# Performance work log

Hardware: AMD Instinct MI355X
Metric: run time of the kernel (lower is better)

The kernel has to match this reference:

```python
import jax, jax.numpy as jnp
import numpy as np

ALPHA = 0.2  # LeakyReLU negative slope
NEG_INF = -9e15


def setup_inputs() -> dict:
    key = jax.random.key(0)
    k1, k2, k3, k4 = jax.random.split(key, 4)
    B, N, F_in, F_out = 8, 2048, 512, 256
    h = jax.random.normal(k1, (B, N, F_in), dtype=jnp.float32)
    adj = jax.random.randint(k2, (B, N, N), 0, 2, dtype=jnp.int32)
    W = jax.random.normal(k3, (F_in, F_out), dtype=jnp.float32) * (1.414 / np.sqrt(F_in))
    a = jax.random.normal(k4, (2 * F_out, 1), dtype=jnp.float32) * (1.414 / np.sqrt(2 * F_out))
    return {"h": h, "adj": adj, "W": W, "a": a}


def reference(h, adj, W, a):
    # Wh: [B, N, F_out]
    Wh = jnp.matmul(h, W)
    F_out = W.shape[1]
    a1 = a[:F_out, 0]   # [F_out] -> source (row i) part
    a2 = a[F_out:, 0]   # [F_out] -> target (col j) part
    # e[b,i,j] = leakyrelu(Wh[b,i]@a1 + Wh[b,j]@a2)  (decomposed concat-attention)
    f1 = jnp.einsum('bnf,f->bn', Wh, a1)  # [B, N]
    f2 = jnp.einsum('bnf,f->bn', Wh, a2)  # [B, N]
    e = f1[:, :, None] + f2[:, None, :]   # [B, N, N]
    e = jnp.where(e > 0, e, ALPHA * e)    # LeakyReLU
    e = jnp.where(adj > 0, e, NEG_INF)
    attention = jax.nn.softmax(e, axis=2)
    # dropout p=0.0 / eval mode: identity
    h_prime = jnp.matmul(attention, Wh)   # [B, N, F_out]
    return jax.nn.elu(h_prime)            # concat=True branch
```

## Files before the change

### kernel.cpp

```cpp
#include <hip/hip_runtime.h>
#include <hip/hip_bf16.h>

#define GAT_ALPHA 0.2f

typedef short bf16x8 __attribute__((ext_vector_type(8)));
typedef float f32x4 __attribute__((ext_vector_type(4)));

__device__ __forceinline__ unsigned f2bf_u(float x) {
  union { float f; unsigned u; } v; v.f = x;
  return (v.u + 0x7fffu + ((v.u >> 16) & 1u)) >> 16;
}
__device__ __forceinline__ unsigned short f2bf(float x) { return (unsigned short)f2bf_u(x); }

__global__ void k_wt(const float* __restrict__ W, unsigned short* __restrict__ WT) {
  int kb = blockIdx.x * 8;
  int f = threadIdx.x;
  bf16x8 o;
#pragma unroll
  for (int i = 0; i < 8; ++i) o[i] = (short)f2bf(W[(kb + i) * 256 + f]);
  *reinterpret_cast<bf16x8*>(WT + f * 512 + kb) = o;
}

__global__ __launch_bounds__(256, 4) void k_gemm1(
    const float* __restrict__ h, const unsigned short* __restrict__ WT,
    const float* __restrict__ avec,
    unsigned short* __restrict__ WhT,
    float* __restrict__ E1p, float* __restrict__ E1n,
    float* __restrict__ E2p, float* __restrict__ E2n)
{
  const int bx = blockIdx.x;
  const int b = bx & 7, ng = bx >> 3;
  const int n0 = ng * 32;
  const int t = threadIdx.x;
  const int lane = t & 63, w = t >> 6;
  const int l15 = lane & 15, q = lane >> 4;

  __shared__ __align__(16) unsigned short Wt[256 * 36];
  __shared__ float f1a[32], f2a[32];
  if (t < 32) { f1a[t] = 0.f; f2a[t] = 0.f; }

  f32x4 acc[4][2];
#pragma unroll
  for (int i = 0; i < 4; ++i)
#pragma unroll
    for (int j = 0; j < 2; ++j) acc[i][j] = (f32x4){0.f, 0.f, 0.f, 0.f};

  const size_t hbase = ((size_t)(b * 2048 + n0)) * 512;

#pragma unroll 2
  for (int k0 = 0; k0 < 512; k0 += 32) {
    bf16x8 af[4];
#pragma unroll
    for (int mt = 0; mt < 4; ++mt)
      af[mt] = *reinterpret_cast<const bf16x8*>(WT + (w * 64 + mt * 16 + l15) * 512 + k0 + q * 8);
    bf16x8 bfr[2];
#pragma unroll
    for (int nt = 0; nt < 2; ++nt) {
      const float* hp = h + hbase + (size_t)(nt * 16 + l15) * 512 + k0 + q * 8;
      float4 x0 = *reinterpret_cast<const float4*>(hp);
      float4 x1 = *reinterpret_cast<const float4*>(hp + 4);
      bf16x8 bb;
      bb[0] = (short)f2bf(x0.x); bb[1] = (short)f2bf(x0.y);
      bb[2] = (short)f2bf(x0.z); bb[3] = (short)f2bf(x0.w);
      bb[4] = (short)f2bf(x1.x); bb[5] = (short)f2bf(x1.y);
      bb[6] = (short)f2bf(x1.z); bb[7] = (short)f2bf(x1.w);
      bfr[nt] = bb;
    }
#pragma unroll
    for (int mt = 0; mt < 4; ++mt)
#pragma unroll
      for (int nt = 0; nt < 2; ++nt)
        acc[mt][nt] = __builtin_amdgcn_mfma_f32_16x16x32_bf16(af[mt], bfr[nt], acc[mt][nt], 0, 0, 0);
  }

  float s1[2] = {0.f, 0.f}, s2[2] = {0.f, 0.f};
#pragma unroll
  for (int mt = 0; mt < 4; ++mt) {
#pragma unroll
    for (int nt = 0; nt < 2; ++nt) {
#pragma unroll
      for (int r = 0; r < 4; ++r) {
        int f = w * 64 + mt * 16 + q * 4 + r;
        float v = acc[mt][nt][r];
        Wt[f * 36 + nt * 16 + l15] = f2bf(v);
        s1[nt] += v * avec[f];
        s2[nt] += v * avec[256 + f];
      }
    }
  }
#pragma unroll
  for (int nt = 0; nt < 2; ++nt) {
    s1[nt] += __shfl_xor(s1[nt], 16); s1[nt] += __shfl_xor(s1[nt], 32);
    s2[nt] += __shfl_xor(s2[nt], 16); s2[nt] += __shfl_xor(s2[nt], 32);
  }
  __syncthreads();
  if (q == 0) {
#pragma unroll
    for (int nt = 0; nt < 2; ++nt) {
      atomicAdd(&f1a[nt * 16 + l15], s1[nt]);
      atomicAdd(&f2a[nt * 16 + l15], s2[nt]);
    }
  }
#pragma unroll
  for (int i = 0; i < 8; ++i) {
    int f = i * 32 + (t >> 3), g = t & 7;
    uint2 v = *reinterpret_cast<const uint2*>(Wt + f * 36 + g * 4);
    *reinterpret_cast<uint2*>(WhT + (size_t)(b * 256 + f) * 2048 + n0 + g * 4) = v;
  }
  __syncthreads();
  if (t < 32) {
    int n = b * 2048 + n0 + t;
    float f1 = f1a[t], f2 = f2a[t];
    E1p[n] = __expf(f1);
    E1n[n] = __expf(GAT_ALPHA * f1);
    E2p[n] = __expf(f2);
    E2n[n] = __expf(GAT_ALPHA * f2);
  }
}

__device__ __forceinline__ void build_frag(
    unsigned short* dst, int4 alo, int4 ahi, float e1p, float e1n,
    float4 epl, float4 eph, float4 enl, float4 enh, float& den)
{
  float p0 = alo.x ? fmaxf(e1p * epl.x, e1n * enl.x) : 0.f;
  float p1 = alo.y ? fmaxf(e1p * epl.y, e1n * enl.y) : 0.f;
  float p2 = alo.z ? fmaxf(e1p * epl.z, e1n * enl.z) : 0.f;
  float p3 = alo.w ? fmaxf(e1p * epl.w, e1n * enl.w) : 0.f;
  float p4 = ahi.x ? fmaxf(e1p * eph.x, e1n * enh.x) : 0.f;
  float p5 = ahi.y ? fmaxf(e1p * eph.y, e1n * enh.y) : 0.f;
  float p6 = ahi.z ? fmaxf(e1p * eph.z, e1n * enh.z) : 0.f;
  float p7 = ahi.w ? fmaxf(e1p * eph.w, e1n * enh.w) : 0.f;
  den += ((p0 + p1) + (p2 + p3)) + ((p4 + p5) + (p6 + p7));
  uint4 pk;
  pk.x = f2bf_u(p0) | (f2bf_u(p1) << 16);
  pk.y = f2bf_u(p2) | (f2bf_u(p3) << 16);
  pk.z = f2bf_u(p4) | (f2bf_u(p5) << 16);
  pk.w = f2bf_u(p6) | (f2bf_u(p7) << 16);
  *reinterpret_cast<uint4*>(dst) = pk;
}

template<int JS>
__global__ __launch_bounds__(512, 4) void k_gat(
    const int* __restrict__ adj, const unsigned short* __restrict__ WhT,
    const float* __restrict__ E1p, const float* __restrict__ E1n,
    const float* __restrict__ E2p, const float* __restrict__ E2n,
    float* __restrict__ num0, float* __restrict__ num1, float* __restrict__ denp)
{
  const int NCH = 16 / JS;
  const int bx = blockIdx.x;
  const int b = bx & 7;
  const int rest = bx >> 3;
  const int js = (JS == 2) ? (rest & 1) : 0;
  const int ig = (JS == 2) ? (rest >> 1) : rest;
  const int i0 = ig * 64;
  const int j00 = js * (NCH * 128);

  const int t = threadIdx.x;
  const int lane = t & 63, w = t >> 6;
  const int l15 = lane & 15, q = lane >> 4;
  const int m = t & 15, qk = (t >> 4) & 3, pp = t >> 6;
  const int rt0 = pp >> 2, ks = pp & 3;
  const int r0 = rt0 * 16 + m, r1 = r0 + 32;
  const int cb = ks * 32 + qk * 8;

  __shared__ __align__(16) unsigned short Pb[2][8192];
  __shared__ float den_l[64];
  if (t < 64) den_l[t] = 0.f;

  const float e1p0 = E1p[b * 2048 + i0 + r0], e1n0 = E1n[b * 2048 + i0 + r0];
  const float e1p1 = E1p[b * 2048 + i0 + r1], e1n1 = E1n[b * 2048 + i0 + r1];
  float d0 = 0.f, d1 = 0.f;

  f32x4 acc[4][2];
#pragma unroll
  for (int i = 0; i < 4; ++i)
#pragma unroll
    for (int j = 0; j < 2; ++j) acc[i][j] = (f32x4){0.f, 0.f, 0.f, 0.f};

  const size_t adj0 = ((size_t)(b * 2048 + i0 + r0)) * 2048 + j00 + cb;
  const size_t adj1 = adj0 + (size_t)32 * 2048;
  const int e2b = b * 2048 + j00 + cb;
  const unsigned short* Wb = WhT + (size_t)(b * 256 + w * 32) * 2048 + j00;

  {
    int4 a0l = *reinterpret_cast<const int4*>(adj + adj0);
    int4 a0h = *reinterpret_cast<const int4*>(adj + adj0 + 4);
    int4 a1l = *reinterpret_cast<const int4*>(adj + adj1);
    int4 a1h = *reinterpret_cast<const int4*>(adj + adj1 + 4);
    float4 epl = *reinterpret_cast<const float4*>(E2p + e2b);
    float4 eph = *reinterpret_cast<const float4*>(E2p + e2b + 4);
    float4 enl = *reinterpret_cast<const float4*>(E2n + e2b);
    float4 enh = *reinterpret_cast<const float4*>(E2n + e2b + 4);
    build_frag(&Pb[0][(pp * 64 + lane) * 8], a0l, a0h, e1p0, e1n0, epl, eph, enl, enh, d0);
    build_frag(&Pb[0][((pp + 8) * 64 + lane) * 8], a1l, a1h, e1p1, e1n1, epl, eph, enl, enh, d1);
  }

  for (int c = 0; c < NCH; ++c) {
    __syncthreads();
    int4 na0l, na0h, na1l, na1h;
    if (c + 1 < NCH) {
      int o = (c + 1) * 128;
      na0l = *reinterpret_cast<const int4*>(adj + adj0 + o);
      na0h = *reinterpret_cast<const int4*>(adj + adj0 + o + 4);
      na1l = *reinterpret_cast<const int4*>(adj + adj1 + o);
      na1h = *reinterpret_cast<const int4*>(adj + adj1 + o + 4);
    }
    bf16x8 bfr[2][4];
#pragma unroll
    for (int ct = 0; ct < 2; ++ct)
#pragma unroll
      for (int k2 = 0; k2 < 4; ++k2)
        bfr[ct][k2] = *reinterpret_cast<const bf16x8*>(
            Wb + (size_t)(ct * 16 + l15) * 2048 + c * 128 + k2 * 32 + q * 8);
    const unsigned short* pb = &Pb[c & 1][0];
#pragma unroll
    for (int k2 = 0; k2 < 4; ++k2) {
      bf16x8 afr[4];
#pragma unroll
      for (int rt = 0; rt < 4; ++rt)
        afr[rt] = *reinterpret_cast<const bf16x8*>(pb + ((rt * 4 + k2) * 64 + lane) * 8);
#pragma unroll
      for (int rt = 0; rt < 4; ++rt)
#pragma unroll
        for (int ct = 0; ct < 2; ++ct)
          acc[rt][ct] = __builtin_amdgcn_mfma_f32_16x16x32_bf16(afr[rt], bfr[ct][k2], acc[rt][ct], 0, 0, 0);
    }
    if (c + 1 < NCH) {
      int o = (c + 1) * 128;
      float4 epl = *reinterpret_cast<const float4*>(E2p + e2b + o);
      float4 eph = *reinterpret_cast<const float4*>(E2p + e2b + o + 4);
      float4 enl = *reinterpret_cast<const float4*>(E2n + e2b + o);
      float4 enh = *reinterpret_cast<const float4*>(E2n + e2b + o + 4);
      unsigned short* wb = &Pb[(c + 1) & 1][0];
      build_frag(wb + (pp * 64 + lane) * 8, na0l, na0h, e1p0, e1n0, epl, eph, enl, enh, d0);
      build_frag(wb + ((pp + 8) * 64 + lane) * 8, na1l, na1h, e1p1, e1n1, epl, eph, enl, enh, d1);
    }
  }

  d0 += __shfl_xor(d0, 16); d0 += __shfl_xor(d0, 32);
  d1 += __shfl_xor(d1, 16); d1 += __shfl_xor(d1, 32);
  if (lane < 16) {
    atomicAdd(&den_l[r0], d0);
    atomicAdd(&den_l[r1], d1);
  }
  __syncthreads();

  float* nout = (JS == 2 && js == 1) ? num1 : num0;
#pragma unroll
  for (int rt = 0; rt < 4; ++rt) {
#pragma unroll
    for (int r = 0; r < 4; ++r) {
      int row = rt * 16 + q * 4 + r;
      size_t ob = ((size_t)(b * 2048 + i0 + row)) * 256 + w * 32;
#pragma unroll
      for (int ct = 0; ct < 2; ++ct)
        nout[ob + ct * 16 + l15] = acc[rt][ct][r];
    }
  }
  if (t < 64) denp[js * 16384 + b * 2048 + i0 + t] = den_l[t];
}

template<int JS>
__global__ __launch_bounds__(256) void k_fin(
    const float* __restrict__ n0p, const float* __restrict__ n1p,
    const float* __restrict__ denp, float* __restrict__ out)
{
  int i = blockIdx.x * 256 + threadIdx.x;
#pragma unroll
  for (int rep = 0; rep < 2; ++rep) {
    int i4 = i + rep * 524288;
    float4 v = reinterpret_cast<const float4*>(n0p)[i4];
    float dn = denp[i4 >> 6];
    if (JS == 2) {
      float4 u = reinterpret_cast<const float4*>(n1p)[i4];
      v.x += u.x; v.y += u.y; v.z += u.z; v.w += u.w;
      dn += denp[16384 + (i4 >> 6)];
    }
    float id = 1.0f / dn;
    float4 o;
    float x;
    x = v.x * id; o.x = x > 0.f ? x : (__expf(x) - 1.f);
    x = v.y * id; o.y = x > 0.f ? x : (__expf(x) - 1.f);
    x = v.z * id; o.z = x > 0.f ? x : (__expf(x) - 1.f);
    x = v.w * id; o.w = x > 0.f ? x : (__expf(x) - 1.f);
    reinterpret_cast<float4*>(out)[i4] = o;
  }
}

extern "C" void kernel_launch(void* const* d_in, const int* in_sizes, int n_in,
                              void* d_out, int out_size, void* d_ws, size_t ws_size,
                              hipStream_t stream) {
  const float* h   = (const float*)d_in[0];
  const int*   adj = (const int*)d_in[1];
  const float* W   = (const float*)d_in[2];
  const float* a   = (const float*)d_in[3];
  float* out = (float*)d_out;

  char* ws = (char*)d_ws;
  unsigned short* WhT = (unsigned short*)ws;
  unsigned short* WT  = (unsigned short*)(ws + 8388608);
  float* E1p  = (float*)(ws + 8388608 + 262144);
  float* E1n  = E1p + 16384;
  float* E2p  = E1n + 16384;
  float* E2n  = E2p + 16384;
  float* denp = E2n + 16384;
  float* num1 = denp + 2 * 16384;

  const size_t need2 = 8388608ull + 262144 + 4 * 65536 + 131072 + 16777216;
  const bool js2 = (ws_size >= need2);

  k_wt<<<dim3(64), dim3(256), 0, stream>>>(W, WT);
  k_gemm1<<<dim3(512), dim3(256), 0, stream>>>(h, WT, a, WhT, E1p, E1n, E2p, E2n);
  if (js2) {
    k_gat<2><<<dim3(512), dim3(512), 0, stream>>>(adj, WhT, E1p, E1n, E2p, E2n, out, num1, denp);
    k_fin<2><<<dim3(2048), dim3(256), 0, stream>>>(out, num1, denp, out);
  } else {
    k_gat<1><<<dim3(256), dim3(512), 0, stream>>>(adj, WhT, E1p, E1n, E2p, E2n, out, num1, denp);
    k_fin<1><<<dim3(2048), dim3(256), 0, stream>>>(out, num1, denp, out);
  }
}
```

Before: 284.6 us.

## Drop split-K GAT path, fuse normalize+ELU epilogue, deepen register prefetch pipelines

The gemm1 loop is rewritten as a fully unrolled register-prefetch pipeline: WT is loaded one step ahead and h two steps ahead. The GAT kernel drops the two-way column split and the separate finalize kernel. Softmax normalization and ELU now run in its epilogue, which saves one launch and the partial-sum round trip through global memory. Its adj/E2 loads are prefetched two chunks ahead and the WhT fragments one chunk ahead. The cost is a grid of only 256 blocks, lower occupancy hints and higher register pressure, which could leave the GPU underfilled.

Measured after the change: 262.3 us. 1.09x faster.

```diff
diff --git a/kernel.cpp b/kernel.cpp
--- a/kernel.cpp
+++ b/kernel.cpp
@@ -21,7 +21,7 @@
   *reinterpret_cast<bf16x8*>(WT + f * 512 + kb) = o;
 }
 
-__global__ __launch_bounds__(256, 4) void k_gemm1(
+__global__ __launch_bounds__(256, 2) void k_gemm1(
     const float* __restrict__ h, const unsigned short* __restrict__ WT,
     const float* __restrict__ avec,
     unsigned short* __restrict__ WhT,
@@ -46,19 +46,41 @@
     for (int j = 0; j < 2; ++j) acc[i][j] = (f32x4){0.f, 0.f, 0.f, 0.f};
 
   const size_t hbase = ((size_t)(b * 2048 + n0)) * 512;
-
-#pragma unroll 2
-  for (int k0 = 0; k0 < 512; k0 += 32) {
-    bf16x8 af[4];
-#pragma unroll
-    for (int mt = 0; mt < 4; ++mt)
-      af[mt] = *reinterpret_cast<const bf16x8*>(WT + (w * 64 + mt * 16 + l15) * 512 + k0 + q * 8);
+  const unsigned short* wtb = WT + (w * 64 + l15) * 512 + q * 8;
+  const float* hrow0 = h + hbase + (size_t)l15 * 512 + q * 8;
+  const float* hrow1 = h + hbase + (size_t)(16 + l15) * 512 + q * 8;
+
+  bf16x8 afA[4], afN[4];
+  float4 hA[4], hB[4], hN[4];
+#pragma unroll
+  for (int mt = 0; mt < 4; ++mt) afA[mt] = *reinterpret_cast<const bf16x8*>(wtb + mt * 16 * 512);
+  hA[0] = *reinterpret_cast<const float4*>(hrow0);
+  hA[1] = *reinterpret_cast<const float4*>(hrow0 + 4);
+  hA[2] = *reinterpret_cast<const float4*>(hrow1);
+  hA[3] = *reinterpret_cast<const float4*>(hrow1 + 4);
+  hB[0] = *reinterpret_cast<const float4*>(hrow0 + 32);
+  hB[1] = *reinterpret_cast<const float4*>(hrow0 + 36);
+  hB[2] = *reinterpret_cast<const float4*>(hrow1 + 32);
+  hB[3] = *reinterpret_cast<const float4*>(hrow1 + 36);
+
+#pragma unroll
+  for (int k = 0; k < 16; ++k) {
+    if (k < 15) {
+      const unsigned short* p = wtb + (k + 1) * 32;
+#pragma unroll
+      for (int mt = 0; mt < 4; ++mt) afN[mt] = *reinterpret_cast<const bf16x8*>(p + mt * 16 * 512);
+    }
+    if (k < 14) {
+      int o = (k + 2) * 32;
+      hN[0] = *reinterpret_cast<const float4*>(hrow0 + o);
+      hN[1] = *reinterpret_cast<const float4*>(hrow0 + o + 4);
+      hN[2] = *reinterpret_cast<const float4*>(hrow1 + o);
+      hN[3] = *reinterpret_cast<const float4*>(hrow1 + o + 4);
+    }
     bf16x8 bfr[2];
 #pragma unroll
     for (int nt = 0; nt < 2; ++nt) {
-      const float* hp = h + hbase + (size_t)(nt * 16 + l15) * 512 + k0 + q * 8;
-      float4 x0 = *reinterpret_cast<const float4*>(hp);
-      float4 x1 = *reinterpret_cast<const float4*>(hp + 4);
+      float4 x0 = hA[nt * 2], x1 = hA[nt * 2 + 1];
       bf16x8 bb;
       bb[0] = (short)f2bf(x0.x); bb[1] = (short)f2bf(x0.y);
       bb[2] = (short)f2bf(x0.z); bb[3] = (short)f2bf(x0.w);
@@ -70,7 +92,15 @@
     for (int mt = 0; mt < 4; ++mt)
 #pragma unroll
       for (int nt = 0; nt < 2; ++nt)
-        acc[mt][nt] = __builtin_amdgcn_mfma_f32_16x16x32_bf16(af[mt], bfr[nt], acc[mt][nt], 0, 0, 0);
+        acc[mt][nt] = __builtin_amdgcn_mfma_f32_16x16x32_bf16(afA[mt], bfr[nt], acc[mt][nt], 0, 0, 0);
+    if (k < 15) {
+#pragma unroll
+      for (int mt = 0; mt < 4; ++mt) afA[mt] = afN[mt];
+#pragma unroll
+      for (int i = 0; i < 4; ++i) hA[i] = hB[i];
+#pragma unroll
+      for (int i = 0; i < 4; ++i) hB[i] = hN[i];
+    }
   }
 
   float s1[2] = {0.f, 0.f}, s2[2] = {0.f, 0.f};
@@ -139,22 +169,15 @@
   *reinterpret_cast<uint4*>(dst) = pk;
 }
 
-template<int JS>
-__global__ __launch_bounds__(512, 4) void k_gat(
+__global__ __launch_bounds__(512, 2) void k_gat(
     const int* __restrict__ adj, const unsigned short* __restrict__ WhT,
     const float* __restrict__ E1p, const float* __restrict__ E1n,
     const float* __restrict__ E2p, const float* __restrict__ E2n,
-    float* __restrict__ num0, float* __restrict__ num1, float* __restrict__ denp)
+    float* __restrict__ out)
 {
-  const int NCH = 16 / JS;
   const int bx = blockIdx.x;
-  const int b = bx & 7;
-  const int rest = bx >> 3;
-  const int js = (JS == 2) ? (rest & 1) : 0;
-  const int ig = (JS == 2) ? (rest >> 1) : rest;
+  const int b = bx & 7, ig = bx >> 3;
   const int i0 = ig * 64;
-  const int j00 = js * (NCH * 128);
-
   const int t = threadIdx.x;
   const int lane = t & 63, w = t >> 6;
   const int l15 = lane & 15, q = lane >> 4;
@@ -177,41 +200,61 @@
 #pragma unroll
     for (int j = 0; j < 2; ++j) acc[i][j] = (f32x4){0.f, 0.f, 0.f, 0.f};
 
-  const size_t adj0 = ((size_t)(b * 2048 + i0 + r0)) * 2048 + j00 + cb;
+  const size_t adj0 = ((size_t)(b * 2048 + i0 + r0)) * 2048 + cb;
   const size_t adj1 = adj0 + (size_t)32 * 2048;
-  const int e2b = b * 2048 + j00 + cb;
-  const unsigned short* Wb = WhT + (size_t)(b * 256 + w * 32) * 2048 + j00;
-
-  {
-    int4 a0l = *reinterpret_cast<const int4*>(adj + adj0);
-    int4 a0h = *reinterpret_cast<const int4*>(adj + adj0 + 4);
-    int4 a1l = *reinterpret_cast<const int4*>(adj + adj1);
-    int4 a1h = *reinterpret_cast<const int4*>(adj + adj1 + 4);
-    float4 epl = *reinterpret_cast<const float4*>(E2p + e2b);
-    float4 eph = *reinterpret_cast<const float4*>(E2p + e2b + 4);
-    float4 enl = *reinterpret_cast<const float4*>(E2n + e2b);
-    float4 enh = *reinterpret_cast<const float4*>(E2n + e2b + 4);
-    build_frag(&Pb[0][(pp * 64 + lane) * 8], a0l, a0h, e1p0, e1n0, epl, eph, enl, enh, d0);
-    build_frag(&Pb[0][((pp + 8) * 64 + lane) * 8], a1l, a1h, e1p1, e1n1, epl, eph, enl, enh, d1);
-  }
-
-  for (int c = 0; c < NCH; ++c) {
-    __syncthreads();
-    int4 na0l, na0h, na1l, na1h;
-    if (c + 1 < NCH) {
-      int o = (c + 1) * 128;
-      na0l = *reinterpret_cast<const int4*>(adj + adj0 + o);
-      na0h = *reinterpret_cast<const int4*>(adj + adj0 + o + 4);
-      na1l = *reinterpret_cast<const int4*>(adj + adj1 + o);
-      na1h = *reinterpret_cast<const int4*>(adj + adj1 + o + 4);
-    }
-    bf16x8 bfr[2][4];
-#pragma unroll
-    for (int ct = 0; ct < 2; ++ct)
-#pragma unroll
-      for (int k2 = 0; k2 < 4; ++k2)
-        bfr[ct][k2] = *reinterpret_cast<const bf16x8*>(
-            Wb + (size_t)(ct * 16 + l15) * 2048 + c * 128 + k2 * 32 + q * 8);
+  const int e2b = b * 2048 + cb;
+  const unsigned short* Wb = WhT + (size_t)(b * 256 + w * 32) * 2048;
+
+  int4 z0l = *reinterpret_cast<const int4*>(adj + adj0);
+  int4 z0h = *reinterpret_cast<const int4*>(adj + adj0 + 4);
+  int4 z1l = *reinterpret_cast<const int4*>(adj + adj1);
+  int4 z1h = *reinterpret_cast<const int4*>(adj + adj1 + 4);
+  float4 zpl = *reinterpret_cast<const float4*>(E2p + e2b);
+  float4 zph = *reinterpret_cast<const float4*>(E2p + e2b + 4);
+  float4 znl = *reinterpret_cast<const float4*>(E2n + e2b);
+  float4 znh = *reinterpret_cast<const float4*>(E2n + e2b + 4);
+  bf16x8 bcur[2][4], bnxt[2][4];
+#pragma unroll
+  for (int ct = 0; ct < 2; ++ct)
+#pragma unroll
+    for (int k2 = 0; k2 < 4; ++k2)
+      bcur[ct][k2] = *reinterpret_cast<const bf16x8*>(
+          Wb + (size_t)(ct * 16 + l15) * 2048 + k2 * 32 + q * 8);
+  int4 A0l = *reinterpret_cast<const int4*>(adj + adj0 + 128);
+  int4 A0h = *reinterpret_cast<const int4*>(adj + adj0 + 132);
+  int4 A1l = *reinterpret_cast<const int4*>(adj + adj1 + 128);
+  int4 A1h = *reinterpret_cast<const int4*>(adj + adj1 + 132);
+  float4 Epl = *reinterpret_cast<const float4*>(E2p + e2b + 128);
+  float4 Eph = *reinterpret_cast<const float4*>(E2p + e2b + 132);
+  float4 Enl = *reinterpret_cast<const float4*>(E2n + e2b + 128);
+  float4 Enh = *reinterpret_cast<const float4*>(E2n + e2b + 132);
+  build_frag(&Pb[0][(pp * 64 + lane) * 8], z0l, z0h, e1p0, e1n0, zpl, zph, znl, znh, d0);
+  build_frag(&Pb[0][((pp + 8) * 64 + lane) * 8], z1l, z1h, e1p1, e1n1, zpl, zph, znl, znh, d1);
+  __syncthreads();
+
+#pragma unroll
+  for (int c = 0; c < 16; ++c) {
+    if (c < 15) {
+      const unsigned short* p = Wb + (c + 1) * 128 + q * 8;
+#pragma unroll
+      for (int ct = 0; ct < 2; ++ct)
+#pragma unroll
+        for (int k2 = 0; k2 < 4; ++k2)
+          bnxt[ct][k2] = *reinterpret_cast<const bf16x8*>(p + (size_t)(ct * 16 + l15) * 2048 + k2 * 32);
+    }
+    int4 nA0l, nA0h, nA1l, nA1h;
+    float4 nEpl, nEph, nEnl, nEnh;
+    if (c < 14) {
+      int o = (c + 2) * 128;
+      nA0l = *reinterpret_cast<const int4*>(adj + adj0 + o);
+      nA0h = *reinterpret_cast<const int4*>(adj + adj0 + o + 4);
+      nA1l = *reinterpret_cast<const int4*>(adj + adj1 + o);
+      nA1h = *reinterpret_cast<const int4*>(adj + adj1 + o + 4);
+      nEpl = *reinterpret_cast<const float4*>(E2p + e2b + o);
+      nEph = *reinterpret_cast<const float4*>(E2p + e2b + o + 4);
+      nEnl = *reinterpret_cast<const float4*>(E2n + e2b + o);
+      nEnh = *reinterpret_cast<const float4*>(E2n + e2b + o + 4);
+    }
     const unsigned short* pb = &Pb[c & 1][0];
 #pragma unroll
     for (int k2 = 0; k2 < 4; ++k2) {
@@ -223,17 +266,23 @@
       for (int rt = 0; rt < 4; ++rt)
 #pragma unroll
         for (int ct = 0; ct < 2; ++ct)
-          acc[rt][ct] = __builtin_amdgcn_mfma_f32_16x16x32_bf16(afr[rt], bfr[ct][k2], acc[rt][ct], 0, 0, 0);
-    }
-    if (c + 1 < NCH) {
-      int o = (c + 1) * 128;
-      float4 epl = *reinterpret_cast<const float4*>(E2p + e2b + o);
-      float4 eph = *reinterpret_cast<const float4*>(E2p + e2b + o + 4);
-      float4 enl = *reinterpret_cast<const float4*>(E2n + e2b + o);
-      float4 enh = *reinterpret_cast<const float4*>(E2n + e2b + o + 4);
+          acc[rt][ct] = __builtin_amdgcn_mfma_f32_16x16x32_bf16(afr[rt], bcur[ct][k2], acc[rt][ct], 0, 0, 0);
+    }
+    if (c < 15) {
       unsigned short* wb = &Pb[(c + 1) & 1][0];
-      build_frag(wb + (pp * 64 + lane) * 8, na0l, na0h, e1p0, e1n0, epl, eph, enl, enh, d0);
-      build_frag(wb + ((pp + 8) * 64 + lane) * 8, na1l, na1h, e1p1, e1n1, epl, eph, enl, enh, d1);
+      build_frag(wb + (pp * 64 + lane) * 8, A0l, A0h, e1p0, e1n0, Epl, Eph, Enl, Enh, d0);
+      build_frag(wb + ((pp + 8) * 64 + lane) * 8, A1l, A1h, e1p1, e1n1, Epl, Eph, Enl, Enh, d1);
+    }
+    if (c < 15) __syncthreads();
+    if (c < 15) {
+#pragma unroll
+      for (int ct = 0; ct < 2; ++ct)
+#pragma unroll
+        for (int k2 = 0; k2 < 4; ++k2) bcur[ct][k2] = bnxt[ct][k2];
+    }
+    if (c < 14) {
+      A0l = nA0l; A0h = nA0h; A1l = nA1l; A1h = nA1h;
+      Epl = nEpl; Eph = nEph; Enl = nEnl; Enh = nEnh;
     }
   }
 
@@ -245,45 +294,20 @@
   }
   __syncthreads();
 
-  float* nout = (JS == 2 && js == 1) ? num1 : num0;
 #pragma unroll
   for (int rt = 0; rt < 4; ++rt) {
 #pragma unroll
     for (int r = 0; r < 4; ++r) {
       int row = rt * 16 + q * 4 + r;
+      float dinv = 1.0f / den_l[row];
       size_t ob = ((size_t)(b * 2048 + i0 + row)) * 256 + w * 32;
 #pragma unroll
-      for (int ct = 0; ct < 2; ++ct)
-        nout[ob + ct * 16 + l15] = acc[rt][ct][r];
-    }
-  }
-  if (t < 64) denp[js * 16384 + b * 2048 + i0 + t] = den_l[t];
-}
-
-template<int JS>
-__global__ __launch_bounds__(256) void k_fin(
-    const float* __restrict__ n0p, const float* __restrict__ n1p,
-    const float* __restrict__ denp, float* __restrict__ out)
-{
-  int i = blockIdx.x * 256 + threadIdx.x;
-#pragma unroll
-  for (int rep = 0; rep < 2; ++rep) {
-    int i4 = i + rep * 524288;
-    float4 v = reinterpret_cast<const float4*>(n0p)[i4];
-    float dn = denp[i4 >> 6];
-    if (JS == 2) {
-      float4 u = reinterpret_cast<const float4*>(n1p)[i4];
-      v.x += u.x; v.y += u.y; v.z += u.z; v.w += u.w;
-      dn += denp[16384 + (i4 >> 6)];
-    }
-    float id = 1.0f / dn;
-    float4 o;
-    float x;
-    x = v.x * id; o.x = x > 0.f ? x : (__expf(x) - 1.f);
-    x = v.y * id; o.y = x > 0.f ? x : (__expf(x) - 1.f);
-    x = v.z * id; o.z = x > 0.f ? x : (__expf(x) - 1.f);
-    x = v.w * id; o.w = x > 0.f ? x : (__expf(x) - 1.f);
-    reinterpret_cast<float4*>(out)[i4] = o;
+      for (int ct = 0; ct < 2; ++ct) {
+        float v = acc[rt][ct][r] * dinv;
+        v = v > 0.f ? v : (__expf(v) - 1.f);
+        out[ob + ct * 16 + l15] = v;
+      }
+    }
   }
 }
 
@@ -303,19 +327,8 @@
   float* E1n  = E1p + 16384;
   float* E2p  = E1n + 16384;
   float* E2n  = E2p + 16384;
-  float* denp = E2n + 16384;
-  float* num1 = denp + 2 * 16384;
-
-  const size_t need2 = 8388608ull + 262144 + 4 * 65536 + 131072 + 16777216;
-  const bool js2 = (ws_size >= need2);
 
   k_wt<<<dim3(64), dim3(256), 0, stream>>>(W, WT);
   k_gemm1<<<dim3(512), dim3(256), 0, stream>>>(h, WT, a, WhT, E1p, E1n, E2p, E2n);
-  if (js2) {
-    k_gat<2><<<dim3(512), dim3(512), 0, stream>>>(adj, WhT, E1p, E1n, E2p, E2n, out, num1, denp);
-    k_fin<2><<<dim3(2048), dim3(256), 0, stream>>>(out, num1, denp, out);
-  } else {
-    k_gat<1><<<dim3(256), dim3(512), 0, stream>>>(adj, WhT, E1p, E1n, E2p, E2n, out, num1, denp);
-    k_fin<1><<<dim3(2048), dim3(256), 0, stream>>>(out, num1, denp, out);
-  }
-}
+  k_gat<<<dim3(256), dim3(512), 0, stream>>>(adj, WhT, E1p, E1n, E2p, E2n, out);
+}
```
